# Kernel optimization log

Measured on AMD Instinct MI355X. Metric: run time of the kernel, lower is better.

Reference implementation:

```python
import jax, jax.numpy as jnp
import numpy as np

EMBED = 1024
HEADS = 16
HEAD_DIM = EMBED // HEADS
N, L = 8, 1024


def setup_inputs() -> dict:
    key = jax.random.key(0)
    ks = jax.random.split(key, 12)
    s = 1.0 / np.sqrt(EMBED)
    return {
        "values": jax.random.normal(ks[0], (N, L, EMBED), jnp.float32),
        "keys": jax.random.normal(ks[1], (N, L, EMBED), jnp.float32),
        "queries": jax.random.normal(ks[2], (N, L, EMBED), jnp.float32),
        "mask": jax.random.randint(ks[3], (N, 1, L, L), 0, 2, jnp.int32),
        "Wv": jax.random.normal(ks[4], (EMBED, EMBED), jnp.float32) * s,
        "bv": jnp.zeros((EMBED,), jnp.float32),
        "Wk": jax.random.normal(ks[5], (EMBED, EMBED), jnp.float32) * s,
        "bk": jnp.zeros((EMBED,), jnp.float32),
        "Wq": jax.random.normal(ks[6], (EMBED, EMBED), jnp.float32) * s,
        "bq": jnp.zeros((EMBED,), jnp.float32),
        "Wo": jax.random.normal(ks[7], (EMBED, EMBED), jnp.float32) * s,
        "bo": jnp.zeros((EMBED,), jnp.float32),
    }


def reference(values, keys, queries, mask, Wv, bv, Wk, bk, Wq, bq, Wo, bo):
    n, q_len = queries.shape[0], queries.shape[1]
    # Linear projections (torch Linear: x @ W.T + b)
    v = values @ Wv.T + bv
    k = keys @ Wk.T + bk
    q = queries @ Wq.T + bq
    # split heads: [N, L, H, D]
    v = v.reshape(n, -1, HEADS, HEAD_DIM)
    k = k.reshape(n, -1, HEADS, HEAD_DIM)
    q = q.reshape(n, q_len, HEADS, HEAD_DIM)
    # energy: [N, H, Q, K]
    energy = jnp.einsum("nqhd,nkhd->nhqk", q, k)
    energy = jnp.where(mask == 0, jnp.float32(-1e20), energy)
    attention = jax.nn.softmax(energy / jnp.sqrt(jnp.float32(EMBED)), axis=3)
    out = jnp.einsum("nhqk,nkhd->nqhd", attention, v).reshape(n, q_len, EMBED)
    return out @ Wo.T + bo
```

## Files before the change

### kernel.cpp

```cpp
#include <hip/hip_runtime.h>
#include <hip/hip_bf16.h>


typedef __attribute__((ext_vector_type(8))) short short8;
typedef __attribute__((ext_vector_type(8))) __bf16 bf16x8;
typedef __attribute__((ext_vector_type(4))) float f32x4;
typedef __attribute__((ext_vector_type(16))) float f32x16;
typedef __attribute__((ext_vector_type(4))) unsigned short ushort4v;

static __device__ __forceinline__ unsigned short f2bf(float x) {
  union { float f; unsigned u; } v; v.f = x;
  unsigned r = v.u + 0x7FFFu + ((v.u >> 16) & 1u);
  return (unsigned short)(r >> 16);
}

static __device__ __forceinline__ f32x4 mfma16(short8 a, short8 b, f32x4 c) {
  return __builtin_amdgcn_mfma_f32_16x16x32_bf16(
      __builtin_bit_cast(bf16x8, a), __builtin_bit_cast(bf16x8, b), c, 0, 0, 0);
}
static __device__ __forceinline__ f32x16 mfma32(short8 a, short8 b, f32x16 c) {
  return __builtin_amdgcn_mfma_f32_32x32x16_bf16(
      __builtin_bit_cast(bf16x8, a), __builtin_bit_cast(bf16x8, b), c, 0, 0, 0);
}

static __device__ __forceinline__ void gll16(const unsigned short* g, unsigned short* l) {
  __builtin_amdgcn_global_load_lds(
      (const __attribute__((address_space(1))) unsigned int*)(const void*)g,
      (__attribute__((address_space(3))) unsigned int*)(void*)l, 16, 0, 0);
}

static __device__ __forceinline__ unsigned cvtpk(float lo, float hi) {
  unsigned r;
  asm("v_cvt_pk_bf16_f32 %0, %1, %2" : "=v"(r) : "v"(lo), "v"(hi));
  return r;
}

static __device__ __forceinline__ void cvt8(const float* __restrict__ in,
                                            unsigned short* __restrict__ out, int i) {
  float4 a = ((const float4*)in)[i * 2];
  float4 b = ((const float4*)in)[i * 2 + 1];
  union { short8 v; unsigned short u[8]; } pk;
  pk.u[0] = f2bf(a.x); pk.u[1] = f2bf(a.y); pk.u[2] = f2bf(a.z); pk.u[3] = f2bf(a.w);
  pk.u[4] = f2bf(b.x); pk.u[5] = f2bf(b.y); pk.u[6] = f2bf(b.z); pk.u[7] = f2bf(b.w);
  ((short8*)out)[i] = pk.v;
}

__global__ __launch_bounds__(256)
void fused_pre(const float* __restrict__ queries, const float* __restrict__ keys,
               const float* __restrict__ values,
               const float* __restrict__ Wq, const float* __restrict__ Wk,
               const float* __restrict__ Wv, const float* __restrict__ Wo,
               const int* __restrict__ mask,
               unsigned short* __restrict__ Xq, unsigned short* __restrict__ Xk,
               unsigned short* __restrict__ Xv,
               unsigned short* __restrict__ W4, unsigned long long* __restrict__ M64)
{
  const int bid = blockIdx.x, tid = threadIdx.x;
  if (bid < 4096) {
    cvt8(queries, Xq, bid * 256 + tid);
  } else if (bid < 8192) {
    cvt8(keys, Xk, (bid - 4096) * 256 + tid);
  } else if (bid < 10240) {
    const int wsel = (bid - 8192) >> 9;
    const float* src = wsel == 0 ? Wq : wsel == 1 ? Wk : wsel == 2 ? Wv : Wo;
    cvt8(src, W4 + wsel * 1048576, ((bid - 8192) & 511) * 256 + tid);
  } else if (bid < 11264) {
    const int lane = tid & 63, wid = tid >> 6;
    const int gw = (bid - 10240) * 4 + wid;
#pragma unroll 4
    for (int j = 0; j < 32; ++j) {
      const int w = gw * 32 + j;
      unsigned long long b = __ballot(mask[(size_t)w * 64 + lane] != 0);
      if (lane == 0) M64[w] = b;
    }
  } else {
    cvt8(values, Xv, (bid - 11264) * 256 + tid);
  }
}

__global__ __launch_bounds__(256)
void cvt_kernel(const float* __restrict__ in, unsigned short* __restrict__ out, int n8)
{
  int i = blockIdx.x * 256 + threadIdx.x;
  if (i >= n8) return;
  cvt8(in, out, i);
}

template<int MODE>
__global__ __launch_bounds__(256)
void gemm_kernel(const unsigned short* __restrict__ A, const unsigned short* __restrict__ B,
                 const float* __restrict__ bias, void* __restrict__ outp, float oscale)
{
  __shared__ alignas(16) unsigned short As[128][32];
  __shared__ alignas(16) unsigned short Bs[128][32];
  const int tid = threadIdx.x, lane = tid & 63, wid = tid >> 6;
  const int l15 = lane & 15, lg = lane >> 4;
  const int j = blockIdx.x >> 3;
  const int bm = (blockIdx.x & 7) * 8 + (j & 7), bn = j >> 3;
  const int wr = (wid >> 1) * 64, wc = (wid & 1) * 64;

  f32x4 acc[4][4] = {};
  const int o = wid * 1024 + lane * 16;
  const unsigned short* gA0 = A + (size_t)(bm * 128 + (o >> 6)) * 1024 + ((o & 63) >> 1);
  const unsigned short* gA1 = gA0 + 64 * 1024;
  const unsigned short* gB0 = B + (size_t)(bn * 128 + (o >> 6)) * 1024 + ((o & 63) >> 1);
  const unsigned short* gB1 = gB0 + 64 * 1024;
  unsigned short* lA0 = &As[0][0] + wid * 512;
  unsigned short* lA1 = lA0 + 2048;
  unsigned short* lB0 = &Bs[0][0] + wid * 512;
  unsigned short* lB1 = lB0 + 2048;

  for (int k0 = 0; k0 < 1024; k0 += 32) {
    __syncthreads();
    gll16(gA0 + k0, lA0); gll16(gA1 + k0, lA1);
    gll16(gB0 + k0, lB0); gll16(gB1 + k0, lB1);
    __syncthreads();
    short8 af[4], bf[4];
#pragma unroll
    for (int f = 0; f < 4; ++f) {
      af[f] = *(const short8*)&As[wr + f * 16 + l15][lg * 8];
      bf[f] = *(const short8*)&Bs[wc + f * 16 + l15][lg * 8];
    }
#pragma unroll
    for (int r = 0; r < 4; ++r)
#pragma unroll
      for (int c = 0; c < 4; ++c)
        acc[r][c] = mfma16(af[r], bf[c], acc[r][c]);
  }

#pragma unroll
  for (int r = 0; r < 4; ++r) {
    const int mb = bm * 128 + wr + r * 16 + lg * 4;
#pragma unroll
    for (int c = 0; c < 4; ++c) {
      const int col = bn * 128 + wc + c * 16 + l15;
      const float bv = bias[col];
      if (MODE == 0) {
        unsigned short* O = (unsigned short*)outp;
#pragma unroll
        for (int i = 0; i < 4; ++i)
          O[(size_t)(mb + i) * 1024 + col] = f2bf((acc[r][c][i] + bv) * oscale);
      } else if (MODE == 1) {
        unsigned short* O = (unsigned short*)outp;
        const int n = mb >> 10, l = mb & 1023, hh = col >> 6, d = col & 63;
        union { ushort4v v; unsigned short u[4]; } pk;
#pragma unroll
        for (int i = 0; i < 4; ++i) pk.u[i] = f2bf(acc[r][c][i] + bv);
        *(ushort4v*)&O[(size_t)((n * 16 + hh) * 64 + d) * 1024 + l] = pk.v;
      } else {
        float* O = (float*)outp;
#pragma unroll
        for (int i = 0; i < 4; ++i)
          O[(size_t)(mb + i) * 1024 + col] = acc[r][c][i] + bv;
      }
    }
  }
}

__global__ __launch_bounds__(256)
void attn_kernel(const unsigned short* __restrict__ Q,
                 const unsigned short* __restrict__ K,
                 const unsigned short* __restrict__ VT,
                 const unsigned long long* __restrict__ M64,
                 unsigned short* __restrict__ AO)
{
  __shared__ alignas(16) unsigned short KV[2][8192];
  const int tid = threadIdx.x, lane = tid & 63, wid = tid >> 6;
  const int l31 = lane & 31, hi = lane >> 5, hi4 = hi * 4;
  const int w = (blockIdx.x & 7) * 128 + (blockIdx.x >> 3);
  const int qt = w & 7, nh = w >> 3, h = nh & 15, n = nh >> 4;
  const int qbase = qt * 128 + wid * 32;

  const unsigned short* src[4];
  unsigned short* dst0[4];
  int tstride;
  if (wid < 2) {
#pragma unroll
    for (int i = 0; i < 4; ++i) {
      const int g = wid * 4 + i, c = g >> 1, kh = g & 1;
      src[i] = K + ((size_t)(n * 1024 + kh * 32 + l31) << 10) + h * 64 + c * 16 + hi * 8;
      dst0[i] = &KV[0][g * 512];
    }
    tstride = 64 * 1024;
  } else {
#pragma unroll
    for (int i = 0; i < 4; ++i) {
      const int g = (wid - 2) * 4 + i, kt = g >> 1, dh = g & 1;
      src[i] = VT + ((size_t)(nh * 64 + dh * 32 + l31) << 10) + kt * 16 + hi * 8;
      dst0[i] = &KV[0][4096 + g * 512];
    }
    tstride = 64;
  }

  short8 qf[4];
#pragma unroll
  for (int c = 0; c < 4; ++c)
    qf[c] = *(const short8*)&Q[(size_t)(n * 1024 + qbase + l31) * 1024 + h * 64 + c * 16 + hi * 8];

  const unsigned long long* Mq = M64 + (size_t)(n * 1024 + qbase + l31) * 16;
  unsigned long long mw = Mq[0], mwn = 0;

  f32x16 oacc0 = {}, oacc1 = {};
  float l_r = 0.f;

#pragma unroll
  for (int i = 0; i < 4; ++i) gll16(src[i], dst0[i]);

  int cur = 0;
#pragma unroll 2
  for (int t = 0; t < 16; ++t) {
    __syncthreads();
    if (t < 15) {
      const size_t off = (size_t)(t + 1) * tstride;
#pragma unroll
      for (int i = 0; i < 4; ++i) gll16(src[i] + off, dst0[i] + (cur ^ 1) * 8192);
      mwn = Mq[t + 1];
    }
    const unsigned short* Kb = &KV[cur][0];

    f32x16 s0 = {}, s1 = {};
    __builtin_amdgcn_s_setprio(1);
#pragma unroll
    for (int c = 0; c < 4; ++c) {
      short8 kf0 = *(const short8*)&Kb[(c * 2 + 0) * 512 + lane * 8];
      short8 kf1 = *(const short8*)&Kb[(c * 2 + 1) * 512 + lane * 8];
      s0 = mfma32(kf0, qf[c], s0);
      s1 = mfma32(kf1, qf[c], s1);
    }
    __builtin_amdgcn_s_setprio(0);

    const unsigned wlo = (unsigned)mw >> hi4;
    const unsigned whi = (unsigned)(mw >> 32) >> hi4;
#pragma unroll
    for (int kt = 0; kt < 2; ++kt) {
      const unsigned wsh = kt ? whi : wlo;
      const f32x16& sv = kt ? s1 : s0;
      float p[16];
      float lsum = 0.f;
#pragma unroll
      for (int r = 0; r < 16; ++r) {
        const float pe = exp2f(sv[r]);
        const int pos = 8 * (r >> 2) + (r & 3);
        const int msk = ((int)(wsh << (31 - pos))) >> 31;
        p[r] = __builtin_bit_cast(float, __builtin_bit_cast(int, pe) & msk);
        lsum += p[r];
      }
      l_r += lsum;
      unsigned u[4][2];
#pragma unroll
      for (int g = 0; g < 4; ++g) {
        u[g][0] = cvtpk(p[4 * g], p[4 * g + 1]);
        u[g][1] = cvtpk(p[4 * g + 2], p[4 * g + 3]);
      }
      short8 pa0, pa1;
#pragma unroll
      for (int m = 0; m < 2; ++m) {
        unsigned a0 = u[2 * m][0], b0 = u[2 * m + 1][0];
        unsigned a1 = u[2 * m][1], b1 = u[2 * m + 1][1];
        asm("v_permlane32_swap_b32 %0, %1" : "+v"(a0), "+v"(b0));
        asm("v_permlane32_swap_b32 %0, %1" : "+v"(a1), "+v"(b1));
        union { unsigned uu[4]; short8 v; } pk;
        pk.uu[0] = a0; pk.uu[1] = a1; pk.uu[2] = b0; pk.uu[3] = b1;
        if (m == 0) pa0 = pk.v; else pa1 = pk.v;
      }
      __builtin_amdgcn_s_setprio(1);
      {
        const int g0 = (kt * 2 + 0) * 2, g1 = (kt * 2 + 1) * 2;
        short8 vf00 = *(const short8*)&Kb[4096 + (g0 + 0) * 512 + lane * 8];
        short8 vf01 = *(const short8*)&Kb[4096 + (g0 + 1) * 512 + lane * 8];
        short8 vf10 = *(const short8*)&Kb[4096 + (g1 + 0) * 512 + lane * 8];
        short8 vf11 = *(const short8*)&Kb[4096 + (g1 + 1) * 512 + lane * 8];
        oacc0 = mfma32(pa0, vf00, oacc0);
        oacc1 = mfma32(pa0, vf01, oacc1);
        oacc0 = mfma32(pa1, vf10, oacc0);
        oacc1 = mfma32(pa1, vf11, oacc1);
      }
      __builtin_amdgcn_s_setprio(0);
    }

    mw = mwn;
    cur ^= 1;
  }

  const float l_tot = l_r + __shfl_xor(l_r, 32);
  const float inv_l = 1.0f / l_tot;
  const int invi = __builtin_bit_cast(int, inv_l);
#pragma unroll
  for (int r = 0; r < 16; ++r) {
    const int qrow = 8 * (r >> 2) + (r & 3) + hi4;
    const float rl = __builtin_bit_cast(float, __builtin_amdgcn_ds_bpermute(qrow * 4, invi));
    const size_t row = (size_t)(n * 1024 + qbase + qrow) * 1024 + h * 64;
    AO[row + l31]      = f2bf(oacc0[r] * rl);
    AO[row + 32 + l31] = f2bf(oacc1[r] * rl);
  }
}

extern "C" void kernel_launch(void* const* d_in, const int* in_sizes, int n_in,
                              void* d_out, int out_size, void* d_ws, size_t ws_size,
                              hipStream_t stream) {
  (void)in_sizes; (void)n_in; (void)out_size;
  const float* values  = (const float*)d_in[0];
  const float* keys    = (const float*)d_in[1];
  const float* queries = (const float*)d_in[2];
  const int*   mask    = (const int*)d_in[3];
  const float* Wv = (const float*)d_in[4];
  const float* bv = (const float*)d_in[5];
  const float* Wk = (const float*)d_in[6];
  const float* bk = (const float*)d_in[7];
  const float* Wq = (const float*)d_in[8];
  const float* bq = (const float*)d_in[9];
  const float* Wo = (const float*)d_in[10];
  const float* bo = (const float*)d_in[11];

  const size_t MB = 1u << 20;
  char* ws = (char*)d_ws;
  unsigned short* R0  = (unsigned short*)(ws);
  unsigned short* R16 = (unsigned short*)(ws + 16 * MB);
  unsigned short* Qb  = (unsigned short*)(ws + 32 * MB);
  unsigned short* Kb  = (unsigned short*)(ws + 48 * MB);
  unsigned short* W4  = (unsigned short*)(ws + 64 * MB);
  unsigned long long* M64 = (unsigned long long*)(ws + 72 * MB);
  unsigned short* Xv  = (unsigned short*)(ws + 73 * MB);
  const bool foldv = ws_size >= 90 * MB;

  const dim3 b256(256);
  const int NX8 = 8 * 1024 * 1024 / 8;
  const float SCFULL = 0.03125f * 1.44269504089f;

  fused_pre<<<dim3(foldv ? 15360 : 11264), b256, 0, stream>>>(
      queries, keys, values, Wq, Wk, Wv, Wo, mask, R0, R16, Xv, W4, M64);
  gemm_kernel<0><<<dim3(512), b256, 0, stream>>>(R0,  W4,               bq, (void*)Qb, SCFULL);
  gemm_kernel<0><<<dim3(512), b256, 0, stream>>>(R16, W4 + 1048576,     bk, (void*)Kb, 1.0f);
  if (!foldv)
    cvt_kernel<<<dim3(4096), b256, 0, stream>>>(values, R0, NX8);
  gemm_kernel<1><<<dim3(512), b256, 0, stream>>>(foldv ? Xv : R0, W4 + 2 * 1048576,
                                                 bv, (void*)R16, 1.0f);
  attn_kernel<<<dim3(1024), b256, 0, stream>>>(Qb, Kb, R16, M64, R0 );
  gemm_kernel<2><<<dim3(512), b256, 0, stream>>>(R0, W4 + 3 * 1048576, bo, d_out, 1.0f);
}
```

Before: 222.6 us.

## Double-buffer GEMM LDS tiles, merge Q/K projections, use bitfield mask extract

The GEMM body now uses two LDS buffers. It prefetches the next K-slice with global-to-LDS loads while computing on the current one, which removes one barrier per iteration. The Q and K projections are merged into a single 1024-block launch so the GPU holds more concurrent work and pays for one less kernel launch. In the attention softmax, the per-element mask bit shift is replaced with a byte select plus sbfe bitfield extract. Doubling the LDS footprint may reduce occupancy, and correctness of the prefetch depends on the barrier waiting for outstanding LDS-bound loads.

```diff
diff --git a/kernel.cpp b/kernel.cpp
--- a/kernel.cpp
+++ b/kernel.cpp
@@ -87,16 +87,17 @@
 }
 
 template<int MODE>
-__global__ __launch_bounds__(256)
-void gemm_kernel(const unsigned short* __restrict__ A, const unsigned short* __restrict__ B,
-                 const float* __restrict__ bias, void* __restrict__ outp, float oscale)
-{
-  __shared__ alignas(16) unsigned short As[128][32];
-  __shared__ alignas(16) unsigned short Bs[128][32];
+static __device__ __forceinline__
+void gemm_body(const unsigned short* __restrict__ A, const unsigned short* __restrict__ B,
+               const float* __restrict__ bias, void* __restrict__ outp,
+               float oscale, int bid)
+{
+  __shared__ alignas(16) unsigned short As[2][4096];
+  __shared__ alignas(16) unsigned short Bs[2][4096];
   const int tid = threadIdx.x, lane = tid & 63, wid = tid >> 6;
   const int l15 = lane & 15, lg = lane >> 4;
-  const int j = blockIdx.x >> 3;
-  const int bm = (blockIdx.x & 7) * 8 + (j & 7), bn = j >> 3;
+  const int j = bid >> 3;
+  const int bm = (bid & 7) * 8 + (j & 7), bn = j >> 3;
   const int wr = (wid >> 1) * 64, wc = (wid & 1) * 64;
 
   f32x4 acc[4][4] = {};
@@ -110,22 +111,32 @@
   unsigned short* lB0 = &Bs[0][0] + wid * 512;
   unsigned short* lB1 = lB0 + 2048;
 
+  gll16(gA0, lA0); gll16(gA1, lA1);
+  gll16(gB0, lB0); gll16(gB1, lB1);
+
+  int cur = 0;
+#pragma unroll 2
   for (int k0 = 0; k0 < 1024; k0 += 32) {
     __syncthreads();
-    gll16(gA0 + k0, lA0); gll16(gA1 + k0, lA1);
-    gll16(gB0 + k0, lB0); gll16(gB1 + k0, lB1);
-    __syncthreads();
+    if (k0 + 32 < 1024) {
+      const int nb = (cur ^ 1) * 4096;
+      gll16(gA0 + k0 + 32, lA0 + nb); gll16(gA1 + k0 + 32, lA1 + nb);
+      gll16(gB0 + k0 + 32, lB0 + nb); gll16(gB1 + k0 + 32, lB1 + nb);
+    }
+    const unsigned short* Ab = &As[cur][0];
+    const unsigned short* Bb = &Bs[cur][0];
     short8 af[4], bf[4];
 #pragma unroll
     for (int f = 0; f < 4; ++f) {
-      af[f] = *(const short8*)&As[wr + f * 16 + l15][lg * 8];
-      bf[f] = *(const short8*)&Bs[wc + f * 16 + l15][lg * 8];
+      af[f] = *(const short8*)&Ab[(wr + f * 16 + l15) * 32 + lg * 8];
+      bf[f] = *(const short8*)&Bb[(wc + f * 16 + l15) * 32 + lg * 8];
     }
 #pragma unroll
     for (int r = 0; r < 4; ++r)
 #pragma unroll
       for (int c = 0; c < 4; ++c)
         acc[r][c] = mfma16(af[r], bf[c], acc[r][c]);
+    cur ^= 1;
   }
 
 #pragma unroll
@@ -158,6 +169,31 @@
 }
 
 __global__ __launch_bounds__(256)
+void gemm_qk(const unsigned short* __restrict__ Xq, const unsigned short* __restrict__ Xk,
+             const unsigned short* __restrict__ W4,
+             const float* __restrict__ bq, const float* __restrict__ bk,
+             unsigned short* __restrict__ Qb, unsigned short* __restrict__ Kb, float scq)
+{
+  const int region = blockIdx.x >> 9;
+  gemm_body<0>(region ? Xk : Xq, W4 + region * 1048576, region ? bk : bq,
+               region ? (void*)Kb : (void*)Qb, region ? 1.0f : scq, blockIdx.x & 511);
+}
+
+__global__ __launch_bounds__(256)
+void gemm_v(const unsigned short* __restrict__ A, const unsigned short* __restrict__ B,
+            const float* __restrict__ bias, void* __restrict__ outp)
+{
+  gemm_body<1>(A, B, bias, outp, 1.0f, blockIdx.x);
+}
+
+__global__ __launch_bounds__(256)
+void gemm_o(const unsigned short* __restrict__ A, const unsigned short* __restrict__ B,
+            const float* __restrict__ bias, void* __restrict__ outp)
+{
+  gemm_body<2>(A, B, bias, outp, 1.0f, blockIdx.x);
+}
+
+__global__ __launch_bounds__(256)
 void attn_kernel(const unsigned short* __restrict__ Q,
                  const unsigned short* __restrict__ K,
                  const unsigned short* __restrict__ VT,
@@ -234,14 +270,17 @@
 #pragma unroll
     for (int kt = 0; kt < 2; ++kt) {
       const unsigned wsh = kt ? whi : wlo;
+      const int gb0 = (int)wsh, gb1 = (int)(wsh >> 8),
+                gb2 = (int)(wsh >> 16), gb3 = (int)(wsh >> 24);
       const f32x16& sv = kt ? s1 : s0;
       float p[16];
       float lsum = 0.f;
 #pragma unroll
       for (int r = 0; r < 16; ++r) {
         const float pe = exp2f(sv[r]);
-        const int pos = 8 * (r >> 2) + (r & 3);
-        const int msk = ((int)(wsh << (31 - pos))) >> 31;
+        const int g = r >> 2;
+        const int gbv = (g == 0) ? gb0 : (g == 1) ? gb1 : (g == 2) ? gb2 : gb3;
+        const int msk = __builtin_amdgcn_sbfe(gbv, r & 3, 1);
         p[r] = __builtin_bit_cast(float, __builtin_bit_cast(int, pe) & msk);
         lsum += p[r];
       }
@@ -329,12 +368,11 @@
 
   fused_pre<<<dim3(foldv ? 15360 : 11264), b256, 0, stream>>>(
       queries, keys, values, Wq, Wk, Wv, Wo, mask, R0, R16, Xv, W4, M64);
-  gemm_kernel<0><<<dim3(512), b256, 0, stream>>>(R0,  W4,               bq, (void*)Qb, SCFULL);
-  gemm_kernel<0><<<dim3(512), b256, 0, stream>>>(R16, W4 + 1048576,     bk, (void*)Kb, 1.0f);
+  gemm_qk<<<dim3(1024), b256, 0, stream>>>(R0, R16, W4, bq, bk, Qb, Kb, SCFULL);
   if (!foldv)
     cvt_kernel<<<dim3(4096), b256, 0, stream>>>(values, R0, NX8);
-  gemm_kernel<1><<<dim3(512), b256, 0, stream>>>(foldv ? Xv : R0, W4 + 2 * 1048576,
-                                                 bv, (void*)R16, 1.0f);
+  gemm_v<<<dim3(512), b256, 0, stream>>>(foldv ? Xv : R0, W4 + 2 * 1048576,
+                                         bv, (void*)R16);
   attn_kernel<<<dim3(1024), b256, 0, stream>>>(Qb, Kb, R16, M64, R0 );
-  gemm_kernel<2><<<dim3(512), b256, 0, stream>>>(R0, W4 + 3 * 1048576, bo, d_out, 1.0f);
-}
+  gemm_o<<<dim3(512), b256, 0, stream>>>(R0, W4 + 3 * 1048576, bo, d_out);
+}
```

After: 228.5 us. 2.7% more time.

## Compute V projection transposed directly and sum softmax denominators via MFMA

Applied to the files above, without the earlier changes.

The V projection GEMM now swaps its operands (weights as A, activations as B), so it writes V^T in an [h*64+d][n*1024+l] layout with row-contiguous stores instead of scattered 4-element transposed stores. The attention kernel's V loads are re-indexed to match. The row-sum of probabilities is now accumulated with an extra MFMA against a ones vector rather than scalar adds plus a cross-lane shuffle and bpermute. This adds MFMA work and accumulator registers in the attention loop, and the denominator is now summed from the bf16-rounded probabilities.

```diff
diff --git a/kernel.cpp b/kernel.cpp
--- a/kernel.cpp
+++ b/kernel.cpp
@@ -6,7 +6,6 @@
 typedef __attribute__((ext_vector_type(8))) __bf16 bf16x8;
 typedef __attribute__((ext_vector_type(4))) float f32x4;
 typedef __attribute__((ext_vector_type(16))) float f32x16;
-typedef __attribute__((ext_vector_type(4))) unsigned short ushort4v;
 
 static __device__ __forceinline__ unsigned short f2bf(float x) {
   union { float f; unsigned u; } v; v.f = x;
@@ -96,7 +95,9 @@
   const int tid = threadIdx.x, lane = tid & 63, wid = tid >> 6;
   const int l15 = lane & 15, lg = lane >> 4;
   const int j = blockIdx.x >> 3;
-  const int bm = (blockIdx.x & 7) * 8 + (j & 7), bn = j >> 3;
+  int bm, bn;
+  if (MODE == 3) { bn = (blockIdx.x & 7) * 8 + (j & 7); bm = j >> 3; }
+  else           { bm = (blockIdx.x & 7) * 8 + (j & 7); bn = j >> 3; }
   const int wr = (wid >> 1) * 64, wc = (wid & 1) * 64;
 
   f32x4 acc[4][4] = {};
@@ -134,20 +135,19 @@
 #pragma unroll
     for (int c = 0; c < 4; ++c) {
       const int col = bn * 128 + wc + c * 16 + l15;
-      const float bv = bias[col];
       if (MODE == 0) {
+        const float bv = bias[col];
         unsigned short* O = (unsigned short*)outp;
 #pragma unroll
         for (int i = 0; i < 4; ++i)
           O[(size_t)(mb + i) * 1024 + col] = f2bf((acc[r][c][i] + bv) * oscale);
-      } else if (MODE == 1) {
+      } else if (MODE == 3) {
         unsigned short* O = (unsigned short*)outp;
-        const int n = mb >> 10, l = mb & 1023, hh = col >> 6, d = col & 63;
-        union { ushort4v v; unsigned short u[4]; } pk;
-#pragma unroll
-        for (int i = 0; i < 4; ++i) pk.u[i] = f2bf(acc[r][c][i] + bv);
-        *(ushort4v*)&O[(size_t)((n * 16 + hh) * 64 + d) * 1024 + l] = pk.v;
+#pragma unroll
+        for (int i = 0; i < 4; ++i)
+          O[(size_t)(mb + i) * 8192 + col] = f2bf(acc[r][c][i] + bias[mb + i]);
       } else {
+        const float bv = bias[col];
         float* O = (float*)outp;
 #pragma unroll
         for (int i = 0; i < 4; ++i)
@@ -186,7 +186,7 @@
 #pragma unroll
     for (int i = 0; i < 4; ++i) {
       const int g = (wid - 2) * 4 + i, kt = g >> 1, dh = g & 1;
-      src[i] = VT + ((size_t)(nh * 64 + dh * 32 + l31) << 10) + kt * 16 + hi * 8;
+      src[i] = VT + (size_t)(h * 64 + dh * 32 + l31) * 8192 + n * 1024 + kt * 16 + hi * 8;
       dst0[i] = &KV[0][4096 + g * 512];
     }
     tstride = 64;
@@ -200,8 +200,10 @@
   const unsigned long long* Mq = M64 + (size_t)(n * 1024 + qbase + l31) * 16;
   unsigned long long mw = Mq[0], mwn = 0;
 
-  f32x16 oacc0 = {}, oacc1 = {};
-  float l_r = 0.f;
+  f32x16 oacc0 = {}, oacc1 = {}, lacc = {};
+  short8 ones;
+#pragma unroll
+  for (int j = 0; j < 8; ++j) ones[j] = (short)0x3F80;
 
 #pragma unroll
   for (int i = 0; i < 4; ++i) gll16(src[i], dst0[i]);
@@ -236,16 +238,13 @@
       const unsigned wsh = kt ? whi : wlo;
       const f32x16& sv = kt ? s1 : s0;
       float p[16];
-      float lsum = 0.f;
 #pragma unroll
       for (int r = 0; r < 16; ++r) {
         const float pe = exp2f(sv[r]);
         const int pos = 8 * (r >> 2) + (r & 3);
         const int msk = ((int)(wsh << (31 - pos))) >> 31;
         p[r] = __builtin_bit_cast(float, __builtin_bit_cast(int, pe) & msk);
-        lsum += p[r];
-      }
-      l_r += lsum;
+      }
       unsigned u[4][2];
 #pragma unroll
       for (int g = 0; g < 4; ++g) {
@@ -272,8 +271,10 @@
         short8 vf11 = *(const short8*)&Kb[4096 + (g1 + 1) * 512 + lane * 8];
         oacc0 = mfma32(pa0, vf00, oacc0);
         oacc1 = mfma32(pa0, vf01, oacc1);
+        lacc  = mfma32(pa0, ones, lacc);
         oacc0 = mfma32(pa1, vf10, oacc0);
         oacc1 = mfma32(pa1, vf11, oacc1);
+        lacc  = mfma32(pa1, ones, lacc);
       }
       __builtin_amdgcn_s_setprio(0);
     }
@@ -282,13 +283,10 @@
     cur ^= 1;
   }
 
-  const float l_tot = l_r + __shfl_xor(l_r, 32);
-  const float inv_l = 1.0f / l_tot;
-  const int invi = __builtin_bit_cast(int, inv_l);
 #pragma unroll
   for (int r = 0; r < 16; ++r) {
     const int qrow = 8 * (r >> 2) + (r & 3) + hi4;
-    const float rl = __builtin_bit_cast(float, __builtin_amdgcn_ds_bpermute(qrow * 4, invi));
+    const float rl = 1.0f / lacc[r];
     const size_t row = (size_t)(n * 1024 + qbase + qrow) * 1024 + h * 64;
     AO[row + l31]      = f2bf(oacc0[r] * rl);
     AO[row + 32 + l31] = f2bf(oacc1[r] * rl);
@@ -329,11 +327,11 @@
 
   fused_pre<<<dim3(foldv ? 15360 : 11264), b256, 0, stream>>>(
       queries, keys, values, Wq, Wk, Wv, Wo, mask, R0, R16, Xv, W4, M64);
-  gemm_kernel<0><<<dim3(512), b256, 0, stream>>>(R0,  W4,               bq, (void*)Qb, SCFULL);
-  gemm_kernel<0><<<dim3(512), b256, 0, stream>>>(R16, W4 + 1048576,     bk, (void*)Kb, 1.0f);
+  gemm_kernel<0><<<dim3(512), b256, 0, stream>>>(R0,  W4,           bq, (void*)Qb, SCFULL);
+  gemm_kernel<0><<<dim3(512), b256, 0, stream>>>(R16, W4 + 1048576, bk, (void*)Kb, 1.0f);
   if (!foldv)
     cvt_kernel<<<dim3(4096), b256, 0, stream>>>(values, R0, NX8);
-  gemm_kernel<1><<<dim3(512), b256, 0, stream>>>(foldv ? Xv : R0, W4 + 2 * 1048576,
+  gemm_kernel<3><<<dim3(512), b256, 0, stream>>>(W4 + 2 * 1048576, foldv ? Xv : R0,
                                                  bv, (void*)R16, 1.0f);
   attn_kernel<<<dim3(1024), b256, 0, stream>>>(Qb, Kb, R16, M64, R0 );
   gemm_kernel<2><<<dim3(512), b256, 0, stream>>>(R0, W4 + 3 * 1048576, bo, d_out, 1.0f);
```

Measured after the change: 217.3 us. 2.4% less time.
